# Optimization experiments

Measured on AMD Instinct MI355X. Metric: run time of the kernel, lower is better.

Reference implementation:

```python
import jax, jax.numpy as jnp
import numpy as np

M, N, D, P, N_kv = 512, 4096, 128, 3584, 1024
H, H_kv = N // D, N_kv // D          # 32 query heads, 8 kv heads
G = H // H_kv                        # group size 4
L = P + M                            # cache length 4096


def setup_inputs() -> dict:
    key = jax.random.key(0)
    ks = jax.random.split(key, 6)
    w_scale = 0.008  # ~0.5/sqrt(N): keeps unscaled exp-softmax logits in fp32 range
    return {
        "X": jax.random.normal(ks[0], (M, N), jnp.float32),
        "W_q": jax.random.normal(ks[1], (N, N), jnp.float32) * w_scale,
        "W_k": jax.random.normal(ks[2], (N, N_kv), jnp.float32) * w_scale,
        "W_v": jax.random.normal(ks[3], (N, N_kv), jnp.float32) * w_scale,
        "cache_K": jax.random.normal(ks[4], (H, L, D), jnp.float32) * 0.02,
        "cache_V": jax.random.normal(ks[5], (H, L, D), jnp.float32) * 0.02,
    }


def reference(X, W_q, W_k, W_v, cache_K, cache_V):
    # fused QKV projection
    W_qkv = jnp.concatenate([W_q, W_k, W_v], axis=1)        # [N, N + 2*N_kv]
    qkv = X @ W_qkv                                          # [M, N + 2*N_kv]
    q = qkv[:, :N].reshape(M, H, D).transpose(1, 0, 2)       # [H, M, D]
    k = qkv[:, N:N + N_kv].reshape(M, H_kv, D).transpose(1, 0, 2)   # [H_kv, M, D]
    v = qkv[:, N + N_kv:].reshape(M, H_kv, D).transpose(1, 0, 2)    # [H_kv, M, D]
    # expand grouped KV heads (repeat_interleave) and append to cache at P
    k_exp = jnp.repeat(k, G, axis=0)                         # [H, M, D]
    v_exp = jnp.repeat(v, G, axis=0)
    Kc = cache_K.at[:, P:P + M, :].set(k_exp)                # [H, L, D]
    Vc = cache_V.at[:, P:P + M, :].set(v_exp)
    # naive (unscaled, non-max-subtracted) softmax attention over full cache
    scores = jnp.einsum('hmd,hld->hml', q, Kc)               # [H, M, L]
    e = jnp.exp(scores)
    weights = e / jnp.sum(e, axis=-1, keepdims=True)
    out = jnp.einsum('hml,hld->hmd', weights, Vc)            # [H, M, D]
    return out.transpose(1, 0, 2).reshape(M, H * D)          # [M, N]
```

## Files before the change

### kernel.cpp

```cpp
#include <hip/hip_runtime.h>

typedef __attribute__((ext_vector_type(8))) short short8;
typedef __attribute__((ext_vector_type(4))) float f32x4;

#define M_   512
#define N_   4096
#define D_   128
#define P_   3584
#define NKV  1024
#define L_   4096
#define H_   32

__device__ __forceinline__ ushort f2bf(float f) {
  union { float f; unsigned u; } v; v.f = f;
  unsigned r = (v.u + 0x7fffu + ((v.u >> 16) & 1u)) >> 16;
  return (ushort)r;
}
__device__ __forceinline__ float bf2f(ushort u) {
  union { unsigned u; float f; } v; v.u = ((unsigned)u) << 16;
  return v.f;
}

__device__ __forceinline__ void gload_lds16(const void* g, void* l) {
  __builtin_amdgcn_global_load_lds(
      (const __attribute__((address_space(1))) void*)g,
      (__attribute__((address_space(3))) void*)l, 16, 0, 0);
}

__global__ __launch_bounds__(256) void xconv(const float* __restrict__ X,
                                             ushort* __restrict__ Xs)
{
  int g = blockIdx.x * 256 + threadIdx.x;
  int row = g >> 9;
  int cir = g & 511;
  int grp = cir >> 3, ch = cir & 7;
  const float* src = &X[(size_t)row * 4096 + cir * 8];
  float4 f0 = *reinterpret_cast<const float4*>(src);
  float4 f1 = *reinterpret_cast<const float4*>(src + 4);
  short8 s;
  s[0] = f2bf(f0.x); s[1] = f2bf(f0.y); s[2] = f2bf(f0.z); s[3] = f2bf(f0.w);
  s[4] = f2bf(f1.x); s[5] = f2bf(f1.y); s[6] = f2bf(f1.z); s[7] = f2bf(f1.w);
  int dcol = grp * 64 + ((ch ^ (row & 7)) * 8);
  *reinterpret_cast<short8*>(&Xs[(size_t)row * 4096 + dcol]) = s;
}

__global__ __launch_bounds__(256) void wtrans(
    const float* __restrict__ Wq, const float* __restrict__ Wk,
    const float* __restrict__ Wv, ushort* __restrict__ Wt)
{
  int bx = blockIdx.x;
  int by = blockIdx.y;
  const float* W; int wcols, c0;
  if (by < 64)      { W = Wq; wcols = 4096; c0 = by * 64; }
  else if (by < 80) { W = Wk; wcols = 1024; c0 = (by - 64) * 64; }
  else              { W = Wv; wcols = 1024; c0 = (by - 80) * 64; }
  int orow0 = by * 64;
  int r0 = bx * 64;
  __shared__ float T[64][65];
  int tid = threadIdx.x;

  #pragma unroll
  for (int i = 0; i < 4; ++i) {
    int r = i * 16 + (tid >> 4);
    int c4 = tid & 15;
    float4 f = *reinterpret_cast<const float4*>(&W[(size_t)(r0 + r) * wcols + c0 + c4 * 4]);
    T[r][c4 * 4 + 0] = f.x; T[r][c4 * 4 + 1] = f.y;
    T[r][c4 * 4 + 2] = f.z; T[r][c4 * 4 + 3] = f.w;
  }
  __syncthreads();

  #pragma unroll
  for (int i = 0; i < 2; ++i) {
    int j = i * 256 + tid;
    int orr = j >> 3;
    int ch = j & 7;
    short8 s;
    #pragma unroll
    for (int e = 0; e < 8; ++e) s[e] = f2bf(T[ch * 8 + e][orr]);
    int orow = orow0 + orr;
    int dstch = ch ^ (orow & 7);
    *reinterpret_cast<short8*>(&Wt[(size_t)orow * 4096 + r0 + dstch * 8]) = s;
  }
}

#define GEMM_STAGE(buf, k0g) do {                                             \
    _Pragma("unroll")                                                         \
    for (int i_ = 0; i_ < 4; ++i_) {                                          \
      int blk_ = w * 4 + i_;                                                  \
      gload_lds16(Asrc + (size_t)(blk_ * 8 + (lane >> 3)) * 4096 + (k0g) + (lane & 7) * 8, \
                  &As[buf][blk_ * 512]);                                      \
    }                                                                         \
    _Pragma("unroll")                                                         \
    for (int i_ = 0; i_ < 4; ++i_) {                                          \
      int blk_ = w * 4 + i_;                                                  \
      gload_lds16(Bsrc + (size_t)(blk_ * 8 + (lane >> 3)) * 4096 + (k0g) + (lane & 7) * 8, \
                  &Bs[buf][blk_ * 512]);                                      \
    }                                                                         \
  } while (0)

__global__ __launch_bounds__(256, 2) void qkv_gemm3(
    const ushort* __restrict__ Xs, const ushort* __restrict__ Wt,
    float* __restrict__ pg)
{
  const int bx = blockIdx.x;
  const int by = blockIdx.y;
  const int bz = blockIdx.z;
  const int tid = threadIdx.x, lane = tid & 63, w = tid >> 6;
  const int wr = w >> 1, wc = w & 1;
  const int m0 = by * 128, n0 = bx * 128;
  const int kb0 = bz * 2048;

  __shared__ ushort As[2][128 * 64];
  __shared__ ushort Bs[2][128 * 64];

  f32x4 acc[4][4];
  #pragma unroll
  for (int m = 0; m < 4; ++m)
    #pragma unroll
    for (int n = 0; n < 4; ++n)
      acc[m][n] = (f32x4){0.f, 0.f, 0.f, 0.f};

  const ushort* Asrc = Xs + (size_t)m0 * 4096;
  const ushort* Bsrc = Wt + (size_t)n0 * 4096;

  GEMM_STAGE(0, kb0);
  __syncthreads();
  int cur = 0;

  for (int kt = 0; kt < 32; ++kt) {
    if (kt + 1 < 32) GEMM_STAGE(cur ^ 1, kb0 + (kt + 1) * 64);
    #pragma unroll
    for (int kk = 0; kk < 2; ++kk) {
      short8 a[4], b[4];
      #pragma unroll
      for (int m = 0; m < 4; ++m) {
        int row = wr * 64 + m * 16 + (lane & 15);
        int ch = (kk * 4 + (lane >> 4)) ^ (row & 7);
        a[m] = *reinterpret_cast<const short8*>(&As[cur][row * 64 + ch * 8]);
      }
      #pragma unroll
      for (int n = 0; n < 4; ++n) {
        int row = wc * 64 + n * 16 + (lane & 15);
        int ch = (kk * 4 + (lane >> 4)) ^ (row & 7);
        b[n] = *reinterpret_cast<const short8*>(&Bs[cur][row * 64 + ch * 8]);
      }
      #pragma unroll
      for (int m = 0; m < 4; ++m)
        #pragma unroll
        for (int n = 0; n < 4; ++n)
          acc[m][n] = __builtin_amdgcn_mfma_f32_16x16x32_bf16(a[m], b[n], acc[m][n], 0, 0, 0);
    }
    __syncthreads();
    cur ^= 1;
  }

  float* dst = pg + (size_t)bz * 512 * 6144;
  #pragma unroll
  for (int m = 0; m < 4; ++m)
    #pragma unroll
    for (int n = 0; n < 4; ++n)
      #pragma unroll
      for (int j = 0; j < 4; ++j) {
        int row = m0 + wr * 64 + m * 16 + (lane >> 4) * 4 + j;
        int col = n0 + wc * 64 + n * 16 + (lane & 15);
        dst[(size_t)row * 6144 + col] = acc[m][n][j];
      }
}

__global__ __launch_bounds__(256) void combine_qk(
    const float* __restrict__ pg, ushort* __restrict__ qb,
    ushort* __restrict__ Kb)
{
  int id = blockIdx.x * 256 + threadIdx.x;
  int m = id / 640;
  int c8 = (id - m * 640) * 8;
  const float* p0 = pg + (size_t)m * 6144 + c8;
  const float* p1 = p0 + (size_t)512 * 6144;
  short8 s;
  #pragma unroll
  for (int e = 0; e < 8; ++e) s[e] = f2bf(p0[e] + p1[e]);
  if (c8 < 4096) {
    *reinterpret_cast<short8*>(&qb[(size_t)m * 4096 + c8]) = s;
  } else {
    int o = c8 - 4096;
    int hk = o >> 7, d0 = o & 127;
    int l = P_ + m;
    int ch = (d0 >> 3) ^ (l & 7);
    #pragma unroll
    for (int g = 0; g < 4; ++g)
      *reinterpret_cast<short8*>(&Kb[((size_t)(hk * 4 + g) * L_ + l) * 128 + ch * 8]) = s;
  }
}

__global__ __launch_bounds__(256) void combine_v(
    const float* __restrict__ pg, ushort* __restrict__ Vtb)
{
  int bz = blockIdx.x;
  int mt = bz & 7, hk = (bz >> 3) & 7, dh = bz >> 6;
  int m0 = mt * 64, d0 = dh * 64;
  int colbase = 5120 + hk * 128 + d0;
  __shared__ float T[64][65];
  int tid = threadIdx.x;
  int r = tid >> 2, q4 = tid & 3;

  #pragma unroll
  for (int i = 0; i < 4; ++i) {
    int c = (q4 * 4 + i) * 4;
    const float* p0 = pg + (size_t)(m0 + r) * 6144 + colbase + c;
    const float* p1 = p0 + (size_t)512 * 6144;
    float4 a = *reinterpret_cast<const float4*>(p0);
    float4 b = *reinterpret_cast<const float4*>(p1);
    T[r][c + 0] = a.x + b.x; T[r][c + 1] = a.y + b.y;
    T[r][c + 2] = a.z + b.z; T[r][c + 3] = a.w + b.w;
  }
  __syncthreads();

  #pragma unroll
  for (int p = 0; p < 2; ++p) {
    int idx = p * 256 + tid;
    int dloc = idx >> 3, cc = idx & 7;
    short8 s;
    #pragma unroll
    for (int e = 0; e < 8; ++e) s[e] = f2bf(T[cc * 8 + e][dloc]);
    int d = d0 + dloc;
    int pc = (cc & 4) | ((cc ^ (d >> 1)) & 3);
    int l0 = P_ + m0;
    #pragma unroll
    for (int g = 0; g < 4; ++g) {
      int h = hk * 4 + g;
      *reinterpret_cast<short8*>(&Vtb[((size_t)h * 128 + d) * (size_t)L_ + l0 + pc * 8]) = s;
    }
  }
}

__global__ __launch_bounds__(256) void kconv(
    const float* __restrict__ cacheK, ushort* __restrict__ Kb)
{
  int h = blockIdx.x, lt = blockIdx.y;
  int tid = threadIdx.x;
  int r = tid >> 4, c = tid & 15;
  int l = lt * 16 + r;
  const float* src = &cacheK[((size_t)h * L_ + l) * 128 + c * 8];
  float4 f0 = *reinterpret_cast<const float4*>(src);
  float4 f1 = *reinterpret_cast<const float4*>(src + 4);
  short8 s;
  s[0] = f2bf(f0.x); s[1] = f2bf(f0.y); s[2] = f2bf(f0.z); s[3] = f2bf(f0.w);
  s[4] = f2bf(f1.x); s[5] = f2bf(f1.y); s[6] = f2bf(f1.z); s[7] = f2bf(f1.w);
  int pc = c ^ (l & 7);
  *reinterpret_cast<short8*>(&Kb[((size_t)h * L_ + l) * 128 + pc * 8]) = s;
}

__global__ __launch_bounds__(256) void vconv(
    const float* __restrict__ cacheV, ushort* __restrict__ Vtb)
{
  int h = blockIdx.x, lt = blockIdx.y, dh = blockIdx.z;
  int l0 = lt * 64, d0 = dh * 64;
  __shared__ float T[64][65];
  int tid = threadIdx.x;
  int r4 = tid >> 4, c = tid & 15;

  #pragma unroll
  for (int p = 0; p < 4; ++p) {
    int r = p * 16 + r4;
    float4 f = *reinterpret_cast<const float4*>(
        &cacheV[((size_t)h * L_ + l0 + r) * 128 + d0 + c * 4]);
    T[r][c * 4 + 0] = f.x; T[r][c * 4 + 1] = f.y;
    T[r][c * 4 + 2] = f.z; T[r][c * 4 + 3] = f.w;
  }
  __syncthreads();

  int dr = tid >> 2, part = tid & 3;
  int d = d0 + dr;
  #pragma unroll
  for (int q = 0; q < 2; ++q) {
    int cc = part * 2 + q;
    short8 s;
    #pragma unroll
    for (int e = 0; e < 8; ++e) s[e] = f2bf(T[cc * 8 + e][dr]);
    int pc = (cc & 4) | ((cc ^ (d >> 1)) & 3);
    *reinterpret_cast<short8*>(&Vtb[((size_t)h * 128 + d) * (size_t)L_ + l0 + pc * 8]) = s;
  }
}

#define ATTN_STAGE(buf, l0g) do {                                             \
    _Pragma("unroll")                                                         \
    for (int it_ = 0; it_ < 2; ++it_)                                         \
      gload_lds16(&Kb[kbase + (size_t)((l0g) + w * 8 + it_ * 4 + (lane >> 4)) * 128 + (lane & 15) * 8], \
                  &Ks[buf][(w * 8 + it_ * 4) * 128]);                         \
    _Pragma("unroll")                                                         \
    for (int it_ = 0; it_ < 2; ++it_)                                         \
      gload_lds16(&Vtb[vbase + (size_t)(w * 32 + it_ * 16 + (lane >> 2)) * (size_t)L_ + (l0g) + (lane & 3) * 8], \
                  &Vt[buf][(w * 32 + it_ * 16) * 32]);                        \
  } while (0)

__global__ __launch_bounds__(256, 2) void gqa_attn6(
    const ushort* __restrict__ qb, const ushort* __restrict__ Kb,
    const ushort* __restrict__ Vtb,
    ushort* __restrict__ pob, float* __restrict__ prs)
{
  const int b = blockIdx.x;
  const int s = b & 7;
  const int j = b >> 3;
  const int qt = j & 3;
  const int h = j >> 2;
  const int tid = threadIdx.x, lane = tid & 63, w = tid >> 6;
  const int lo16 = lane & 15, hi = lane >> 4;

  __shared__ ushort Ks[2][32 * 128];
  __shared__ ushort Vt[2][128 * 32];
  __shared__ ushort PsT[128 * 32];

  short8 qreg[2][4];
  #pragma unroll
  for (int rg = 0; rg < 2; ++rg) {
    int qrow = qt * 128 + w * 32 + rg * 16 + lo16;
    #pragma unroll
    for (int kk = 0; kk < 4; ++kk)
      qreg[rg][kk] = *reinterpret_cast<const short8*>(
          &qb[(size_t)qrow * 4096 + h * 128 + (kk * 4 + hi) * 8]);
  }

  f32x4 o[2][8];
  #pragma unroll
  for (int rg = 0; rg < 2; ++rg)
    #pragma unroll
    for (int n = 0; n < 8; ++n)
      o[rg][n] = (f32x4){0.f, 0.f, 0.f, 0.f};
  float rs[2] = {0.f, 0.f};

  const size_t kbase = ((size_t)h * L_ + s * 512) * 128;
  const size_t vbase = (size_t)h * 128 * (size_t)L_ + s * 512;

  ATTN_STAGE(0, 0);
  __syncthreads();
  int cur = 0;

  for (int t = 0; t < 16; ++t) {
    if (t + 1 < 16) ATTN_STAGE(cur ^ 1, (t + 1) * 32);

    f32x4 sc[2][2];
    #pragma unroll
    for (int mb = 0; mb < 2; ++mb)
      #pragma unroll
      for (int rg = 0; rg < 2; ++rg)
        sc[mb][rg] = (f32x4){0.f, 0.f, 0.f, 0.f};
    __builtin_amdgcn_s_setprio(1);
    #pragma unroll
    for (int kk = 0; kk < 4; ++kk) {
      short8 a[2];
      #pragma unroll
      for (int mb = 0; mb < 2; ++mb) {
        int row = mb * 16 + lo16;
        int ch = (kk * 4 + hi) ^ (row & 7);
        a[mb] = *reinterpret_cast<const short8*>(&Ks[cur][row * 128 + ch * 8]);
      }
      #pragma unroll
      for (int mb = 0; mb < 2; ++mb)
        #pragma unroll
        for (int rg = 0; rg < 2; ++rg)
          sc[mb][rg] = __builtin_amdgcn_mfma_f32_16x16x32_bf16(a[mb], qreg[rg][kk], sc[mb][rg], 0, 0, 0);
    }
    __builtin_amdgcn_s_setprio(0);

    #pragma unroll
    for (int mb = 0; mb < 2; ++mb)
      #pragma unroll
      for (int rg = 0; rg < 2; ++rg) {
        float e0 = __expf(sc[mb][rg][0]);
        float e1 = __expf(sc[mb][rg][1]);
        float e2 = __expf(sc[mb][rg][2]);
        float e3 = __expf(sc[mb][rg][3]);
        rs[rg] += (e0 + e1) + (e2 + e3);
        ushort4 u; u.x = f2bf(e0); u.y = f2bf(e1); u.z = f2bf(e2); u.w = f2bf(e3);
        int q = w * 32 + rg * 16 + lo16;
        int ch = mb * 2 + (hi >> 1);
        int slot = ch ^ ((q >> 1) & 3);
        *reinterpret_cast<ushort4*>(&PsT[q * 32 + slot * 8 + (hi & 1) * 4]) = u;
      }

    __builtin_amdgcn_s_setprio(1);
    {
      short8 b8[8];
      #pragma unroll
      for (int n = 0; n < 8; ++n) {
        int d = n * 16 + lo16;
        int ch = hi ^ ((d >> 1) & 3);
        b8[n] = *reinterpret_cast<const short8*>(&Vt[cur][d * 32 + ch * 8]);
      }
      #pragma unroll
      for (int rg = 0; rg < 2; ++rg) {
        int q = w * 32 + rg * 16 + lo16;
        int sl = hi ^ ((q >> 1) & 3);
        short8 a = *reinterpret_cast<const short8*>(&PsT[q * 32 + sl * 8]);
        #pragma unroll
        for (int n = 0; n < 8; ++n)
          o[rg][n] = __builtin_amdgcn_mfma_f32_16x16x32_bf16(a, b8[n], o[rg][n], 0, 0, 0);
      }
    }
    __builtin_amdgcn_s_setprio(0);

    __syncthreads();
    cur ^= 1;
  }

  float rsum[2];
  #pragma unroll
  for (int rg = 0; rg < 2; ++rg) {
    float v = rs[rg];
    v += __shfl_xor(v, 16, 64);
    v += __shfl_xor(v, 32, 64);
    rsum[rg] = v;
  }

  const size_t pbase = (size_t)(s * 32 + h) * 512;
  #pragma unroll
  for (int rg = 0; rg < 2; ++rg)
    #pragma unroll
    for (int n = 0; n < 8; ++n)
      #pragma unroll
      for (int j2 = 0; j2 < 4; ++j2) {
        int row = qt * 128 + w * 32 + rg * 16 + hi * 4 + j2;
        pob[(pbase + row) * 128 + n * 16 + lo16] = f2bf(o[rg][n][j2]);
      }
  if (hi == 0) {
    #pragma unroll
    for (int rg = 0; rg < 2; ++rg) {
      int row = qt * 128 + w * 32 + rg * 16 + lo16;
      prs[pbase + row] = rsum[rg];
    }
  }
}

__global__ __launch_bounds__(256) void reduce_out(
    const ushort* __restrict__ pob, const float* __restrict__ prs,
    float* __restrict__ out)
{
  int id = blockIdx.x * 256 + threadIdx.x;
  int m = id >> 10, dq = id & 1023;
  int h = dq >> 5, d4 = dq & 31;
  float4 acc = {0.f, 0.f, 0.f, 0.f};
  float rsum = 0.f;
  #pragma unroll
  for (int s = 0; s < 8; ++s) {
    size_t base = (size_t)(s * 32 + h) * 512 + m;
    ushort4 v = *reinterpret_cast<const ushort4*>(&pob[base * 128 + d4 * 4]);
    acc.x += bf2f(v.x); acc.y += bf2f(v.y); acc.z += bf2f(v.z); acc.w += bf2f(v.w);
    rsum += prs[base];
  }
  float inv = 1.f / rsum;
  float4 r; r.x = acc.x * inv; r.y = acc.y * inv; r.z = acc.z * inv; r.w = acc.w * inv;
  *reinterpret_cast<float4*>(&out[(size_t)m * 4096 + dq * 4]) = r;
}

extern "C" void kernel_launch(void* const* d_in, const int* in_sizes, int n_in,
                              void* d_out, int out_size, void* d_ws, size_t ws_size,
                              hipStream_t stream) {
  const float* X  = (const float*)d_in[0];
  const float* Wq = (const float*)d_in[1];
  const float* Wk = (const float*)d_in[2];
  const float* Wv = (const float*)d_in[3];
  const float* cK = (const float*)d_in[4];
  const float* cV = (const float*)d_in[5];
  float* out = (float*)d_out;

  ushort* qb  = (ushort*)d_ws;
  ushort* Xs  = qb  + (size_t)M_ * N_;
  ushort* Kb  = Xs  + (size_t)M_ * N_;
  ushort* Vtb = Kb  + (size_t)H_ * L_ * D_;
  float*  prs = (float*)(Vtb + (size_t)H_ * L_ * D_);
  ushort* Wt  = (ushort*)(prs + 8 * 32 * 512);
  float*  pg  = (float*)(Wt + (size_t)6144 * 4096);
  ushort* pob = Wt;

  xconv<<<1024, 256, 0, stream>>>(X, Xs);
  wtrans<<<dim3(64, 96), 256, 0, stream>>>(Wq, Wk, Wv, Wt);
  qkv_gemm3<<<dim3(48, 4, 2), 256, 0, stream>>>(Xs, Wt, pg);
  combine_qk<<<1280, 256, 0, stream>>>(pg, qb, Kb);
  combine_v<<<128, 256, 0, stream>>>(pg, Vtb);
  kconv<<<dim3(32, 224), 256, 0, stream>>>(cK, Kb);
  vconv<<<dim3(32, 56, 2), 256, 0, stream>>>(cV, Vtb);
  gqa_attn6<<<1024, 256, 0, stream>>>(qb, Kb, Vtb, pob, prs);
  reduce_out<<<2048, 256, 0, stream>>>(pob, prs, out);
}
```

Before: 178.1 us.

## Deepen attention K/V prefetch to four LDS buffers with vmcnt-based waits

The attention kernel moves from a double-buffered to a quad-buffered K/V LDS ring that keeps two tiles in flight. It replaces __syncthreads with explicit s_waitcnt vmcnt plus s_barrier and fully unrolls the 16-tile loop. The goal is to hide global-load latency better behind the MFMA work. In exchange, K/V LDS use doubles, which may reduce occupancy, and correctness now depends on the hand-counted vmcnt values and on PsT reuse between tiles without a full barrier.

New measurement: 179.3 us. No clear change (+0.7%).

```diff
diff --git a/kernel.cpp b/kernel.cpp
--- a/kernel.cpp
+++ b/kernel.cpp
@@ -293,7 +293,68 @@
                   &Vt[buf][(w * 32 + it_ * 16) * 32]);                        \
   } while (0)
 
-__global__ __launch_bounds__(256, 2) void gqa_attn6(
+#define ATTN_TILE(bufc) do {                                                  \
+    f32x4 sc[2][2];                                                           \
+    _Pragma("unroll")                                                         \
+    for (int mb = 0; mb < 2; ++mb)                                            \
+      _Pragma("unroll")                                                       \
+      for (int rg = 0; rg < 2; ++rg)                                          \
+        sc[mb][rg] = (f32x4){0.f, 0.f, 0.f, 0.f};                             \
+    __builtin_amdgcn_s_setprio(1);                                            \
+    _Pragma("unroll")                                                         \
+    for (int kk = 0; kk < 4; ++kk) {                                          \
+      short8 a[2];                                                            \
+      _Pragma("unroll")                                                       \
+      for (int mb = 0; mb < 2; ++mb) {                                        \
+        int row = mb * 16 + lo16;                                             \
+        int ch = (kk * 4 + hi) ^ (row & 7);                                   \
+        a[mb] = *reinterpret_cast<const short8*>(&Ks[bufc][row * 128 + ch * 8]); \
+      }                                                                       \
+      _Pragma("unroll")                                                       \
+      for (int mb = 0; mb < 2; ++mb)                                          \
+        _Pragma("unroll")                                                     \
+        for (int rg = 0; rg < 2; ++rg)                                        \
+          sc[mb][rg] = __builtin_amdgcn_mfma_f32_16x16x32_bf16(a[mb], qreg[rg][kk], sc[mb][rg], 0, 0, 0); \
+    }                                                                         \
+    __builtin_amdgcn_s_setprio(0);                                            \
+    _Pragma("unroll")                                                         \
+    for (int mb = 0; mb < 2; ++mb)                                            \
+      _Pragma("unroll")                                                       \
+      for (int rg = 0; rg < 2; ++rg) {                                        \
+        float e0 = __expf(sc[mb][rg][0]);                                     \
+        float e1 = __expf(sc[mb][rg][1]);                                     \
+        float e2 = __expf(sc[mb][rg][2]);                                     \
+        float e3 = __expf(sc[mb][rg][3]);                                     \
+        rs[rg] += (e0 + e1) + (e2 + e3);                                      \
+        ushort4 u; u.x = f2bf(e0); u.y = f2bf(e1); u.z = f2bf(e2); u.w = f2bf(e3); \
+        int q = w * 32 + rg * 16 + lo16;                                      \
+        int ch = mb * 2 + (hi >> 1);                                          \
+        int slot = ch ^ ((q >> 1) & 3);                                       \
+        *reinterpret_cast<ushort4*>(&PsT[q * 32 + slot * 8 + (hi & 1) * 4]) = u; \
+      }                                                                       \
+    __builtin_amdgcn_s_setprio(1);                                            \
+    {                                                                         \
+      short8 b8[8];                                                           \
+      _Pragma("unroll")                                                       \
+      for (int n = 0; n < 8; ++n) {                                           \
+        int d = n * 16 + lo16;                                                \
+        int ch = hi ^ ((d >> 1) & 3);                                         \
+        b8[n] = *reinterpret_cast<const short8*>(&Vt[bufc][d * 32 + ch * 8]); \
+      }                                                                       \
+      _Pragma("unroll")                                                       \
+      for (int rg = 0; rg < 2; ++rg) {                                        \
+        int q = w * 32 + rg * 16 + lo16;                                      \
+        int sl = hi ^ ((q >> 1) & 3);                                         \
+        short8 a = *reinterpret_cast<const short8*>(&PsT[q * 32 + sl * 8]);   \
+        _Pragma("unroll")                                                     \
+        for (int n = 0; n < 8; ++n)                                           \
+          o[rg][n] = __builtin_amdgcn_mfma_f32_16x16x32_bf16(a, b8[n], o[rg][n], 0, 0, 0); \
+      }                                                                       \
+    }                                                                         \
+    __builtin_amdgcn_s_setprio(0);                                            \
+  } while (0)
+
+__global__ __launch_bounds__(256, 2) void gqa_attn7(
     const ushort* __restrict__ qb, const ushort* __restrict__ Kb,
     const ushort* __restrict__ Vtb,
     ushort* __restrict__ pob, float* __restrict__ prs)
@@ -306,8 +367,8 @@
   const int tid = threadIdx.x, lane = tid & 63, w = tid >> 6;
   const int lo16 = lane & 15, hi = lane >> 4;
 
-  __shared__ ushort Ks[2][32 * 128];
-  __shared__ ushort Vt[2][128 * 32];
+  __shared__ ushort Ks[4][32 * 128];
+  __shared__ ushort Vt[4][128 * 32];
   __shared__ ushort PsT[128 * 32];
 
   short8 qreg[2][4];
@@ -332,76 +393,21 @@
   const size_t vbase = (size_t)h * 128 * (size_t)L_ + s * 512;
 
   ATTN_STAGE(0, 0);
-  __syncthreads();
-  int cur = 0;
-
-  for (int t = 0; t < 16; ++t) {
-    if (t + 1 < 16) ATTN_STAGE(cur ^ 1, (t + 1) * 32);
-
-    f32x4 sc[2][2];
-    #pragma unroll
-    for (int mb = 0; mb < 2; ++mb)
-      #pragma unroll
-      for (int rg = 0; rg < 2; ++rg)
-        sc[mb][rg] = (f32x4){0.f, 0.f, 0.f, 0.f};
-    __builtin_amdgcn_s_setprio(1);
-    #pragma unroll
-    for (int kk = 0; kk < 4; ++kk) {
-      short8 a[2];
-      #pragma unroll
-      for (int mb = 0; mb < 2; ++mb) {
-        int row = mb * 16 + lo16;
-        int ch = (kk * 4 + hi) ^ (row & 7);
-        a[mb] = *reinterpret_cast<const short8*>(&Ks[cur][row * 128 + ch * 8]);
-      }
-      #pragma unroll
-      for (int mb = 0; mb < 2; ++mb)
-        #pragma unroll
-        for (int rg = 0; rg < 2; ++rg)
-          sc[mb][rg] = __builtin_amdgcn_mfma_f32_16x16x32_bf16(a[mb], qreg[rg][kk], sc[mb][rg], 0, 0, 0);
-    }
-    __builtin_amdgcn_s_setprio(0);
-
-    #pragma unroll
-    for (int mb = 0; mb < 2; ++mb)
-      #pragma unroll
-      for (int rg = 0; rg < 2; ++rg) {
-        float e0 = __expf(sc[mb][rg][0]);
-        float e1 = __expf(sc[mb][rg][1]);
-        float e2 = __expf(sc[mb][rg][2]);
-        float e3 = __expf(sc[mb][rg][3]);
-        rs[rg] += (e0 + e1) + (e2 + e3);
-        ushort4 u; u.x = f2bf(e0); u.y = f2bf(e1); u.z = f2bf(e2); u.w = f2bf(e3);
-        int q = w * 32 + rg * 16 + lo16;
-        int ch = mb * 2 + (hi >> 1);
-        int slot = ch ^ ((q >> 1) & 3);
-        *reinterpret_cast<ushort4*>(&PsT[q * 32 + slot * 8 + (hi & 1) * 4]) = u;
-      }
-
-    __builtin_amdgcn_s_setprio(1);
-    {
-      short8 b8[8];
-      #pragma unroll
-      for (int n = 0; n < 8; ++n) {
-        int d = n * 16 + lo16;
-        int ch = hi ^ ((d >> 1) & 3);
-        b8[n] = *reinterpret_cast<const short8*>(&Vt[cur][d * 32 + ch * 8]);
-      }
-      #pragma unroll
-      for (int rg = 0; rg < 2; ++rg) {
-        int q = w * 32 + rg * 16 + lo16;
-        int sl = hi ^ ((q >> 1) & 3);
-        short8 a = *reinterpret_cast<const short8*>(&PsT[q * 32 + sl * 8]);
-        #pragma unroll
-        for (int n = 0; n < 8; ++n)
-          o[rg][n] = __builtin_amdgcn_mfma_f32_16x16x32_bf16(a, b8[n], o[rg][n], 0, 0, 0);
-      }
-    }
-    __builtin_amdgcn_s_setprio(0);
-
-    __syncthreads();
-    cur ^= 1;
-  }
+  ATTN_STAGE(1, 32);
+  asm volatile("s_waitcnt vmcnt(4)" ::: "memory");
+  __builtin_amdgcn_s_barrier();
+
+  #pragma unroll
+  for (int t = 0; t < 14; ++t) {
+    ATTN_STAGE((t + 2) & 3, (t + 2) * 32);
+    ATTN_TILE(t & 3);
+    asm volatile("s_waitcnt vmcnt(4)" ::: "memory");
+    __builtin_amdgcn_s_barrier();
+  }
+  ATTN_TILE(2);
+  asm volatile("s_waitcnt vmcnt(0)" ::: "memory");
+  __builtin_amdgcn_s_barrier();
+  ATTN_TILE(3);
 
   float rsum[2];
   #pragma unroll
@@ -479,6 +485,6 @@
   combine_v<<<128, 256, 0, stream>>>(pg, Vtb);
   kconv<<<dim3(32, 224), 256, 0, stream>>>(cK, Kb);
   vconv<<<dim3(32, 56, 2), 256, 0, stream>>>(cV, Vtb);
-  gqa_attn6<<<1024, 256, 0, stream>>>(qb, Kb, Vtb, pob, prs);
+  gqa_attn7<<<1024, 256, 0, stream>>>(qb, Kb, Vtb, pob, prs);
   reduce_out<<<2048, 256, 0, stream>>>(pob, prs, out);
 }
```
